# Kernel optimization log

Measured on AMD Instinct MI355X. Metric: run time of the kernel, lower is better.

The kernel has to match this reference:

```python
import jax, jax.numpy as jnp
import numpy as np

E = 8        # number of part experts
D_IN = 3     # coordinate dim
H = 256      # hidden width (3 hidden layers)
D_OUT = 1


def setup_inputs() -> dict:
    key = jax.random.key(0)
    ks = jax.random.split(key, 9)
    # coords in [-1, 1]
    coords = jax.random.uniform(ks[0], (100000, D_IN), jnp.float32, -1.0, 1.0)
    def glorot(k, shape):
        fan_in, fan_out = shape[-2], shape[-1]
        s = jnp.sqrt(2.0 / (fan_in + fan_out)).astype(jnp.float32)
        return jax.random.normal(k, shape, jnp.float32) * s
    W0 = glorot(ks[1], (E, D_IN, H)); b0 = jnp.zeros((E, H), jnp.float32)
    W1 = glorot(ks[2], (E, H, H));    b1 = jnp.zeros((E, H), jnp.float32)
    W2 = glorot(ks[3], (E, H, H));    b2 = jnp.zeros((E, H), jnp.float32)
    W3 = glorot(ks[4], (E, H, D_OUT)); b3 = jnp.zeros((E, D_OUT), jnp.float32)
    return {"coords": coords, "W0": W0, "b0": b0, "W1": W1, "b1": b1,
            "W2": W2, "b2": b2, "W3": W3, "b3": b3}


def reference(coords, W0, b0, W1, b1, W2, b2, W3, b3):
    # All E experts consume the SAME coords; batch them as grouped GEMMs.
    # h: [E, N, H]
    h = jax.nn.relu(jnp.einsum('nd,edh->enh', coords, W0) + b0[:, None, :])
    h = jax.nn.relu(jnp.einsum('enh,ehk->enk', h, W1) + b1[:, None, :])
    h = jax.nn.relu(jnp.einsum('enh,ehk->enk', h, W2) + b2[:, None, :])
    expert_out = jnp.einsum('enh,eho->eno', h, W3) + b3[:, None, :]  # [E, N, 1]
    # torch.stack(expert_tensors).max(dim=0).values
    max_occ = jnp.max(expert_out, axis=0)  # [N, 1]
    return max_occ
```

## Files before the change

kernel.cpp:

```cpp
#include <hip/hip_runtime.h>
#include <hip/hip_bf16.h>

#define NE 8
#define HD 256
#define NT 64
#define NTHREADS 256
#define WPITCH 32
#define SLICE_ELEMS (HD * WPITCH)

typedef __attribute__((ext_vector_type(8))) short short8;
typedef __attribute__((ext_vector_type(4))) float f32x4;

__device__ __forceinline__ unsigned short f2bf_u16(float f) {
    union { __hip_bfloat16 b; unsigned short u; } v;
    v.b = __float2bfloat16(f);
    return v.u;
}
__device__ __forceinline__ unsigned int pack2bf(float lo, float hi) {
    return (unsigned int)f2bf_u16(lo) | ((unsigned int)f2bf_u16(hi) << 16);
}
__device__ __forceinline__ void bfsplit(float v, unsigned short& hi, unsigned short& lo) {
    hi = f2bf_u16(v);
    union { unsigned int u; float f; } c; c.u = ((unsigned int)hi) << 16;
    lo = f2bf_u16(v - c.f);
}
__device__ __forceinline__ int swz(int row, int col) {
    return row * HD + (col ^ ((row & 7) << 3));
}

__global__ void prep_weights(const float* __restrict__ W1, const float* __restrict__ W2,
                             unsigned short* __restrict__ W1p, unsigned short* __restrict__ W2p) {
    int idx = blockIdx.x * blockDim.x + threadIdx.x;
    const int TOT = NE * 8 * SLICE_ELEMS;
    if (idx >= TOT) return;
    int kk = idx & 31;
    int n  = (idx >> 5) & 255;
    int s  = (idx >> 13) & 7;
    int e  = idx >> 16;
    int k = s * 32 + kk;
    W1p[idx] = f2bf_u16(W1[(e * HD + k) * HD + n]);
    W2p[idx] = f2bf_u16(W2[(e * HD + k) * HD + n]);
}

__global__ void prep_w0(const float* __restrict__ W0, const float* __restrict__ b0,
                        unsigned short* __restrict__ W0k) {
    int idx = blockIdx.x * blockDim.x + threadIdx.x;
    if (idx >= NE * HD) return;
    int n = idx & 255, e = idx >> 8;
    float wx = W0[(e*3+0)*HD + n], wy = W0[(e*3+1)*HD + n], wz = W0[(e*3+2)*HD + n];
    float bb = b0[e*HD + n];
    unsigned short xh,xl,yh,yl,zh,zl,bh,bl;
    bfsplit(wx,xh,xl); bfsplit(wy,yh,yl); bfsplit(wz,zh,zl); bfsplit(bb,bh,bl);
    unsigned short s[32] = {xh,xh,xl, yh,yh,yl, zh,zh,zl, bh,bl};
    unsigned short* dst = W0k + idx * 32;
    #pragma unroll
    for (int i = 0; i < 32; ++i) dst[i] = s[i];
}

__device__ __forceinline__ void stage_slice(const unsigned short* __restrict__ gsrc,
                                            unsigned short* lbase, int g, int lane) {
    const char* gp = (const char*)gsrc + g * 4096 + lane * 16;
    char* l = (char*)lbase + g * 4096;
    #pragma unroll
    for (int i = 0; i < 4; ++i)
        __builtin_amdgcn_global_load_lds(
            (const __attribute__((address_space(1))) unsigned int*)(gp + i * 1024),
            (__attribute__((address_space(3))) unsigned int*)(l + i * 1024),
            16, 0, 0);
}

#define KSLICE_BODY(CURBUF, K0)                                                              \
    {                                                                                        \
        const unsigned short* Ar = (CURBUF) + (g*64 + l15) * WPITCH + kg*8;                  \
        short8 af0 = *(const short8*)(Ar + 0*16*WPITCH);                                     \
        short8 af1 = *(const short8*)(Ar + 1*16*WPITCH);                                     \
        short8 af2 = *(const short8*)(Ar + 2*16*WPITCH);                                     \
        short8 af3 = *(const short8*)(Ar + 3*16*WPITCH);                                     \
        const int k0 = (K0) + kg*8;                                                          \
        _Pragma("unroll")                                                                    \
        for (int nt = 0; nt < 4; ++nt) {                                                     \
            short8 bf = *(const short8*)(Act + swz(nt*16 + l15, k0));                        \
            acc[0][nt] = __builtin_amdgcn_mfma_f32_16x16x32_bf16(af0, bf, acc[0][nt], 0,0,0);\
            acc[1][nt] = __builtin_amdgcn_mfma_f32_16x16x32_bf16(af1, bf, acc[1][nt], 0,0,0);\
            acc[2][nt] = __builtin_amdgcn_mfma_f32_16x16x32_bf16(af2, bf, acc[2][nt], 0,0,0);\
            acc[3][nt] = __builtin_amdgcn_mfma_f32_16x16x32_bf16(af3, bf, acc[3][nt], 0,0,0);\
        }                                                                                    \
    }

#define ACC_CLEAR()                                           \
    _Pragma("unroll")                                         \
    for (int mt = 0; mt < 4; ++mt)                            \
        _Pragma("unroll")                                     \
        for (int nt = 0; nt < 4; ++nt)                        \
            acc[mt][nt] = (f32x4){0.f, 0.f, 0.f, 0.f};

__global__ __launch_bounds__(NTHREADS, 3) void moe_expert(
    const float* __restrict__ coords, int npts,
    const unsigned short* __restrict__ W0k, const float* __restrict__ b1,
    const unsigned short* __restrict__ W1p,
    const unsigned short* __restrict__ W2p, const float* __restrict__ b2,
    const float* __restrict__ W3, const float* __restrict__ b3,
    float* __restrict__ ws)
{
    __shared__ __align__(16) unsigned short Act[NT * HD];
    __shared__ __align__(16) unsigned short Wb[SLICE_ELEMS];
    __shared__ __align__(16) unsigned char aux[NT * 32 * 2];
    unsigned short* cbufK = (unsigned short*)aux;
    float* pscr = (float*)aux;

    const int t = threadIdx.x;
    const int lane = t & 63;
    const int g = t >> 6;
    const int l15 = lane & 15;
    const int kg = lane >> 4;
    const int e = blockIdx.x & 7;
    const int p0 = (blockIdx.x >> 3) * NT;

    const unsigned short* W0e = W0k + e * SLICE_ELEMS;
    const unsigned short* W1e = W1p + e * 8 * SLICE_ELEMS;
    const unsigned short* W2e = W2p + e * 8 * SLICE_ELEMS;

    stage_slice(W0e, Wb, g, lane);
    if (t < NT) {
        int p = p0 + t;
        int pc = p < npts ? p : npts - 1;
        float x = coords[pc*3], y = coords[pc*3+1], z = coords[pc*3+2];
        unsigned short xh,xl,yh,yl,zh,zl;
        bfsplit(x,xh,xl); bfsplit(y,yh,yl); bfsplit(z,zh,zl);
        const unsigned short ONE = 0x3F80;
        union { unsigned short s[32]; uint4 q[4]; } pk;
        #pragma unroll
        for (int i = 0; i < 32; ++i) pk.s[i] = 0;
        pk.s[0]=xh; pk.s[1]=xl; pk.s[2]=xh;
        pk.s[3]=yh; pk.s[4]=yl; pk.s[5]=yh;
        pk.s[6]=zh; pk.s[7]=zl; pk.s[8]=zh;
        pk.s[9]=ONE; pk.s[10]=ONE;
        uint4* dst = (uint4*)(cbufK + t * 32);
        dst[0]=pk.q[0]; dst[1]=pk.q[1]; dst[2]=pk.q[2]; dst[3]=pk.q[3];
    }
    f32x4 b1v[4];
    #pragma unroll
    for (int mt = 0; mt < 4; ++mt)
        b1v[mt] = *(const f32x4*)(b1 + e*HD + g*64 + mt*16 + kg*4);
    __syncthreads();

    f32x4 acc[4][4];
    ACC_CLEAR()

    {
        const unsigned short* Ar = Wb + (g*64 + l15) * WPITCH + kg*8;
        short8 af0 = *(const short8*)(Ar + 0*16*WPITCH);
        short8 af1 = *(const short8*)(Ar + 1*16*WPITCH);
        short8 af2 = *(const short8*)(Ar + 2*16*WPITCH);
        short8 af3 = *(const short8*)(Ar + 3*16*WPITCH);
        #pragma unroll
        for (int nt = 0; nt < 4; ++nt) {
            short8 bf = *(const short8*)(cbufK + (nt*16 + l15) * 32 + kg*8);
            acc[0][nt] = __builtin_amdgcn_mfma_f32_16x16x32_bf16(af0, bf, acc[0][nt], 0,0,0);
            acc[1][nt] = __builtin_amdgcn_mfma_f32_16x16x32_bf16(af1, bf, acc[1][nt], 0,0,0);
            acc[2][nt] = __builtin_amdgcn_mfma_f32_16x16x32_bf16(af2, bf, acc[2][nt], 0,0,0);
            acc[3][nt] = __builtin_amdgcn_mfma_f32_16x16x32_bf16(af3, bf, acc[3][nt], 0,0,0);
        }
        #pragma unroll
        for (int mt = 0; mt < 4; ++mt)
            #pragma unroll
            for (int nt = 0; nt < 4; ++nt) {
                const int p = nt*16 + l15;
                const int n0 = g*64 + mt*16 + kg*4;
                unsigned int lo = pack2bf(fmaxf(acc[mt][nt][0], 0.f),
                                          fmaxf(acc[mt][nt][1], 0.f));
                unsigned int hi = pack2bf(fmaxf(acc[mt][nt][2], 0.f),
                                          fmaxf(acc[mt][nt][3], 0.f));
                *(uint2*)(Act + swz(p, n0)) = make_uint2(lo, hi);
            }
    }
    __syncthreads();
    stage_slice(W1e, Wb, g, lane);
    __syncthreads();

    ACC_CLEAR()
    #pragma unroll
    for (int s = 0; s < 8; ++s) {
        KSLICE_BODY(Wb, s*32)
        __syncthreads();
        if (s < 7) {
            stage_slice(W1e + (s+1) * SLICE_ELEMS, Wb, g, lane);
            __syncthreads();
        }
    }
    stage_slice(W2e, Wb, g, lane);
    #pragma unroll
    for (int mt = 0; mt < 4; ++mt) {
        const int n0 = g*64 + mt*16 + kg*4;
        const f32x4 bb = b1v[mt];
        #pragma unroll
        for (int nt = 0; nt < 4; ++nt) {
            const int p = nt*16 + l15;
            unsigned int lo = pack2bf(fmaxf(acc[mt][nt][0] + bb[0], 0.f),
                                      fmaxf(acc[mt][nt][1] + bb[1], 0.f));
            unsigned int hi = pack2bf(fmaxf(acc[mt][nt][2] + bb[2], 0.f),
                                      fmaxf(acc[mt][nt][3] + bb[3], 0.f));
            *(uint2*)(Act + swz(p, n0)) = make_uint2(lo, hi);
        }
    }
    __syncthreads();

    ACC_CLEAR()
    #pragma unroll
    for (int s = 0; s < 8; ++s) {
        KSLICE_BODY(Wb, s*32)
        if (s < 7) {
            __syncthreads();
            stage_slice(W2e + (s+1) * SLICE_ELEMS, Wb, g, lane);
            __syncthreads();
        }
    }

    {
        f32x4 bbv[4], w3v[4];
        #pragma unroll
        for (int mt = 0; mt < 4; ++mt) {
            const int nb = g*64 + mt*16 + kg*4;
            bbv[mt] = *(const f32x4*)(b2 + e*HD + nb);
            w3v[mt] = *(const f32x4*)(W3 + e*HD + nb);
        }
        __syncthreads();
        #pragma unroll
        for (int nt = 0; nt < 4; ++nt) {
            float s = 0.f;
            #pragma unroll
            for (int mt = 0; mt < 4; ++mt)
                #pragma unroll
                for (int r = 0; r < 4; ++r)
                    s += fmaxf(acc[mt][nt][r] + bbv[mt][r], 0.f) * w3v[mt][r];
            s += __shfl_xor(s, 16);
            s += __shfl_xor(s, 32);
            if (kg == 0) pscr[(nt*16 + l15) * 4 + g] = s;
        }
    }
    __syncthreads();
    if (t < NT) {
        f32x4 v = *(const f32x4*)(pscr + t * 4);
        int p = p0 + t;
        if (p < npts) ws[e * npts + p] = v[0] + v[1] + v[2] + v[3] + b3[e];
    }
}

__global__ void moe_reduce(const float* __restrict__ ws, float* __restrict__ out, int npts) {
    int p = blockIdx.x * 256 + threadIdx.x;
    if (p >= npts) return;
    float m = ws[p];
    #pragma unroll
    for (int e = 1; e < NE; ++e) m = fmaxf(m, ws[e * npts + p]);
    out[p] = m;
}

extern "C" void kernel_launch(void* const* d_in, const int* in_sizes, int n_in,
                              void* d_out, int out_size, void* d_ws, size_t ws_size,
                              hipStream_t stream) {
    const float* coords = (const float*)d_in[0];
    const float* W0 = (const float*)d_in[1];
    const float* b0 = (const float*)d_in[2];
    const float* W1 = (const float*)d_in[3];
    const float* b1 = (const float*)d_in[4];
    const float* W2 = (const float*)d_in[5];
    const float* b2 = (const float*)d_in[6];
    const float* W3 = (const float*)d_in[7];
    const float* b3 = (const float*)d_in[8];
    const int npts = in_sizes[0] / 3;

    unsigned short* W1p = (unsigned short*)d_ws;
    unsigned short* W2p = W1p + NE * 8 * SLICE_ELEMS;
    unsigned short* W0k = W2p + NE * 8 * SLICE_ELEMS;
    float* eout = (float*)(W0k + NE * SLICE_ELEMS);

    const int PREP_TOT = NE * 8 * SLICE_ELEMS;
    prep_weights<<<(PREP_TOT + 255) / 256, 256, 0, stream>>>(W1, W2, W1p, W2p);
    prep_w0<<<(NE * HD + 255) / 256, 256, 0, stream>>>(W0, b0, W0k);

    int ntiles = (npts + NT - 1) / NT;
    moe_expert<<<ntiles * NE, NTHREADS, 0, stream>>>(
        coords, npts, W0k, b1, W1p, W2p, b2, W3, b3, eout);

    moe_reduce<<<(npts + 255) / 256, 256, 0, stream>>>(eout, (float*)d_out, npts);
}
```

Before: 244.2 us.

## Read weight fragments directly from global memory instead of LDS staging

Removes the LDS weight staging buffer and the per-slice global_load_lds copies with their barriers. MFMA A-operands are now read directly from global memory, relying on L1/L2 caching. The freed LDS and the raised launch-bounds occupancy hint aim to allow more resident blocks. In exchange, global load latency now sits inside the MFMA loop without explicit prefetching.

```diff
diff --git a/kernel.cpp b/kernel.cpp
--- a/kernel.cpp
+++ b/kernel.cpp
@@ -57,21 +57,9 @@
     for (int i = 0; i < 32; ++i) dst[i] = s[i];
 }
 
-__device__ __forceinline__ void stage_slice(const unsigned short* __restrict__ gsrc,
-                                            unsigned short* lbase, int g, int lane) {
-    const char* gp = (const char*)gsrc + g * 4096 + lane * 16;
-    char* l = (char*)lbase + g * 4096;
-    #pragma unroll
-    for (int i = 0; i < 4; ++i)
-        __builtin_amdgcn_global_load_lds(
-            (const __attribute__((address_space(1))) unsigned int*)(gp + i * 1024),
-            (__attribute__((address_space(3))) unsigned int*)(l + i * 1024),
-            16, 0, 0);
-}
-
-#define KSLICE_BODY(CURBUF, K0)                                                              \
+#define KSLICE_BODY(WSRC, K0)                                                                \
     {                                                                                        \
-        const unsigned short* Ar = (CURBUF) + (g*64 + l15) * WPITCH + kg*8;                  \
+        const unsigned short* Ar = (WSRC) + (g*64 + l15) * WPITCH + kg*8;                    \
         short8 af0 = *(const short8*)(Ar + 0*16*WPITCH);                                     \
         short8 af1 = *(const short8*)(Ar + 1*16*WPITCH);                                     \
         short8 af2 = *(const short8*)(Ar + 2*16*WPITCH);                                     \
@@ -94,7 +82,7 @@
         for (int nt = 0; nt < 4; ++nt)                        \
             acc[mt][nt] = (f32x4){0.f, 0.f, 0.f, 0.f};
 
-__global__ __launch_bounds__(NTHREADS, 3) void moe_expert(
+__global__ __launch_bounds__(NTHREADS, 4) void moe_expert(
     const float* __restrict__ coords, int npts,
     const unsigned short* __restrict__ W0k, const float* __restrict__ b1,
     const unsigned short* __restrict__ W1p,
@@ -103,7 +91,6 @@
     float* __restrict__ ws)
 {
     __shared__ __align__(16) unsigned short Act[NT * HD];
-    __shared__ __align__(16) unsigned short Wb[SLICE_ELEMS];
     __shared__ __align__(16) unsigned char aux[NT * 32 * 2];
     unsigned short* cbufK = (unsigned short*)aux;
     float* pscr = (float*)aux;
@@ -120,7 +107,6 @@
     const unsigned short* W1e = W1p + e * 8 * SLICE_ELEMS;
     const unsigned short* W2e = W2p + e * 8 * SLICE_ELEMS;
 
-    stage_slice(W0e, Wb, g, lane);
     if (t < NT) {
         int p = p0 + t;
         int pc = p < npts ? p : npts - 1;
@@ -148,7 +134,7 @@
     ACC_CLEAR()
 
     {
-        const unsigned short* Ar = Wb + (g*64 + l15) * WPITCH + kg*8;
+        const unsigned short* Ar = W0e + (g*64 + l15) * WPITCH + kg*8;
         short8 af0 = *(const short8*)(Ar + 0*16*WPITCH);
         short8 af1 = *(const short8*)(Ar + 1*16*WPITCH);
         short8 af2 = *(const short8*)(Ar + 2*16*WPITCH);
@@ -175,20 +161,14 @@
             }
     }
     __syncthreads();
-    stage_slice(W1e, Wb, g, lane);
-    __syncthreads();
 
     ACC_CLEAR()
     #pragma unroll
     for (int s = 0; s < 8; ++s) {
-        KSLICE_BODY(Wb, s*32)
-        __syncthreads();
-        if (s < 7) {
-            stage_slice(W1e + (s+1) * SLICE_ELEMS, Wb, g, lane);
-            __syncthreads();
-        }
-    }
-    stage_slice(W2e, Wb, g, lane);
+        KSLICE_BODY(W1e + s * SLICE_ELEMS, s*32)
+    }
+    __syncthreads();
+
     #pragma unroll
     for (int mt = 0; mt < 4; ++mt) {
         const int n0 = g*64 + mt*16 + kg*4;
@@ -208,12 +188,7 @@
     ACC_CLEAR()
     #pragma unroll
     for (int s = 0; s < 8; ++s) {
-        KSLICE_BODY(Wb, s*32)
-        if (s < 7) {
-            __syncthreads();
-            stage_slice(W2e + (s+1) * SLICE_ELEMS, Wb, g, lane);
-            __syncthreads();
-        }
+        KSLICE_BODY(W2e + s * SLICE_ELEMS, s*32)
     }
 
     {
@@ -224,7 +199,6 @@
             bbv[mt] = *(const f32x4*)(b2 + e*HD + nb);
             w3v[mt] = *(const f32x4*)(W3 + e*HD + nb);
         }
-        __syncthreads();
         #pragma unroll
         for (int nt = 0; nt < 4; ++nt) {
             float s = 0.f;
```

Measured after the change: 245.8 us. No clear change (+0.7%).
